# Optimization experiments

Measured on AMD Instinct MI355X. Metric: run time of the kernel, lower is better.

Reference implementation:

```python
import jax, jax.numpy as jnp
import numpy as np

N_NODES = 50000
N_EDGES = 500000
LATENT = 128
MULS = (64, 32, 16)      # multiplicities for l=0,1,2
DIMS = (1, 3, 5)         # 2l+1
FEAT_OFF = (0, 64, 160)  # feature column offset per l
FEAT_DIM = 240
WIG_OFF = (0, 1, 4)      # wigner block offset per l
D_TOT = 9


def _e3nn_linear(x, W0, b0, W1, W2):
    # e3nn Linear: per-l multiplicity mixing, 1/sqrt(mul_in) path norm, bias only on l=0 scalars
    s = x[:, 0:64] @ (W0 / 8.0) + b0                                                   # l=0
    v = jnp.einsum('nmd,mk->nkd', x[:, 64:160].reshape(-1, 32, 3), W1 / jnp.sqrt(32.0)).reshape(-1, 96)
    t = jnp.einsum('nmd,mk->nkd', x[:, 160:240].reshape(-1, 16, 5), W2 / 4.0).reshape(-1, 80)
    return jnp.concatenate([s, v, t], axis=1)


def setup_inputs():
    key = jax.random.key(0)
    ks = iter(jax.random.split(key, 32))
    f32 = jnp.float32
    def lin(i, o):
        return jax.random.normal(next(ks), (i, o), f32) / np.float32(np.sqrt(i))
    inp = {}
    inp['node_features'] = jax.random.normal(next(ks), (N_NODES, FEAT_DIM), f32)
    inp['active_edge_vector'] = jax.random.normal(next(ks), (N_EDGES, 3), f32)
    inp['active_edge_index'] = jax.random.randint(next(ks), (2, N_EDGES), 0, N_NODES)
    inp['wigner_D_all'] = jax.random.normal(next(ks), (N_EDGES, D_TOT, D_TOT), f32)
    # lin_center / lin_neighbor (e3nn Linear per-l weights, scalar bias)
    inp['Wc0'] = lin(64, 64); inp['bc0'] = jnp.zeros((64,), f32)
    inp['Wc1'] = lin(32, 32); inp['Wc2'] = lin(16, 16)
    inp['Wn0'] = lin(64, 64); inp['bn0'] = jnp.zeros((64,), f32)
    inp['Wn1'] = lin(32, 32); inp['Wn2'] = lin(16, 16)
    # sim_linears per l: in_dim = total_mul * (2l+1)
    inp['Ws0'] = lin(64, LATENT);  inp['bs0'] = jnp.zeros((LATENT,), f32)
    inp['Ws1'] = lin(96, LATENT);  inp['bs1'] = jnp.zeros((LATENT,), f32)
    inp['Ws2'] = lin(80, LATENT);  inp['bs2'] = jnp.zeros((LATENT,), f32)
    # final_mlp: Linear(3*LATENT, 2*LATENT) -> SiLU -> Linear(2*LATENT, LATENT)
    inp['Wf1'] = lin(3 * LATENT, 2 * LATENT); inp['bf1'] = jnp.zeros((2 * LATENT,), f32)
    inp['Wf2'] = lin(2 * LATENT, LATENT);     inp['bf2'] = jnp.zeros((LATENT,), f32)
    return inp


def reference(node_features, active_edge_vector, active_edge_index, wigner_D_all,
              Wc0, bc0, Wc1, Wc2, Wn0, bn0, Wn1, Wn2,
              Ws0, bs0, Ws1, bs1, Ws2, bs2, Wf1, bf1, Wf2, bf2):
    # rot_n_feat_ is an exact copy of node_features in the original forward
    center = _e3nn_linear(node_features, Wc0, bc0, Wc1, Wc2)[active_edge_index[0]]    # (E, 240)
    neigh = _e3nn_linear(node_features, Wn0, bn0, Wn1, Wn2)[active_edge_index[1]]     # (E, 240)
    sim_w = ((Ws0, bs0), (Ws1, bs1), (Ws2, bs2))
    latent_list = []
    for l in range(3):
        mul, d, fo = MULS[l], DIMS[l], FEAT_OFF[l]
        cf = center[:, fo:fo + mul * d].reshape(-1, mul, d)   # (E, mul, 2l+1)
        nf = neigh[:, fo:fo + mul * d].reshape(-1, mul, d)
        if l > 0:
            wo = WIG_OFF[l]
            rot = wigner_D_all[:, wo:wo + d, wo:wo + d]       # (E, d, d) per-l wigner block
            cf = jnp.einsum('emd,edq->emq', cf, rot)
            nf = jnp.einsum('emd,edq->emq', nf, rot)
        sim = (cf * nf).reshape(cf.shape[0], -1)              # (E, mul*d)
        W, b = sim_w[l]
        latent_list.append(jax.nn.silu(sim @ W + b))          # (E, LATENT)
    fused = jnp.concatenate(latent_list, axis=1)              # stack(dim=1)+reshape == concat
    h = jax.nn.silu(fused @ Wf1 + bf1)
    return h @ Wf2 + bf2                                      # (E, LATENT)
```

## Files before the change

kernel.cpp:

```cpp
#include <hip/hip_runtime.h>
#include <hip/hip_fp16.h>
#include <math.h>


#define NFEAT 240

typedef _Float16 f16;
typedef _Float16 f16x8 __attribute__((ext_vector_type(8)));
typedef float f32x4 __attribute__((ext_vector_type(4)));

__device__ __forceinline__ float silu_f(float x) {
    return x / (1.0f + __expf(-x));
}

__device__ __forceinline__ int frag_idx(int s, int e, int kk) {
    return ((s * 2 + (e >> 4)) * 64 + (((kk >> 3) << 4) | (e & 15))) * 8 + (kk & 7);
}

template <bool F32>
__global__ void node_kernel(const float* __restrict__ x,
                            const float* __restrict__ Wc0, const float* __restrict__ bc0,
                            const float* __restrict__ Wc1, const float* __restrict__ Wc2,
                            const float* __restrict__ Wn0, const float* __restrict__ bn0,
                            const float* __restrict__ Wn1, const float* __restrict__ Wn2,
                            void* __restrict__ Cp, void* __restrict__ Np,
                            int n_nodes)
{
    int t = blockIdx.x * blockDim.x + threadIdx.x;
    int total = n_nodes * NFEAT;
    if (t >= total) return;
    int n = t / NFEAT;
    int j = t - n * NFEAT;
    const float* xr = x + (size_t)n * NFEAT;
    float ac = 0.f, an = 0.f;
    if (j < 64) {
        #pragma unroll 8
        for (int m = 0; m < 64; ++m) {
            float xv = xr[m];
            ac = fmaf(xv, Wc0[m * 64 + j], ac);
            an = fmaf(xv, Wn0[m * 64 + j], an);
        }
        ac = ac * 0.125f + bc0[j];
        an = an * 0.125f + bn0[j];
    } else if (j < 160) {
        int s = j - 64; int k = s / 3; int d = s - 3 * k;
        #pragma unroll 8
        for (int m = 0; m < 32; ++m) {
            float xv = xr[64 + m * 3 + d];
            ac = fmaf(xv, Wc1[m * 32 + k], ac);
            an = fmaf(xv, Wn1[m * 32 + k], an);
        }
        const float s32 = 0.17677669529663687f;
        ac *= s32; an *= s32;
    } else {
        int s = j - 160; int k = s / 5; int d = s - 5 * k;
        #pragma unroll 8
        for (int m = 0; m < 16; ++m) {
            float xv = xr[160 + m * 5 + d];
            ac = fmaf(xv, Wc2[m * 16 + k], ac);
            an = fmaf(xv, Wn2[m * 16 + k], an);
        }
        ac *= 0.25f; an *= 0.25f;
    }
    if (F32) {
        ((float*)Cp)[t] = ac;
        ((float*)Np)[t] = an;
    } else {
        ((__half*)Cp)[t] = __float2half(ac);
        ((__half*)Np)[t] = __float2half(an);
    }
}

__global__ void pack_kernel(const float* __restrict__ Ws0, const float* __restrict__ Ws1,
                            const float* __restrict__ Ws2, const float* __restrict__ Wf1,
                            const float* __restrict__ Wf2, f16* __restrict__ P)
{
    int idx = blockIdx.x * 256 + threadIdx.x;
    if (idx >= 163840) return;
    int lane = (idx >> 3) & 63;
    int i = idx & 7;
    int kc = ((lane >> 4) << 3) + i;
    int nl = lane & 15;
    float v;
    if (idx < 32768) {
        int fi = idx >> 9; int s = fi >> 3; int nt = fi & 7;
        int l = (s < 2) ? 0 : ((s < 5) ? 1 : 2);
        int s0 = (l == 0) ? 0 : ((l == 1) ? 2 : 5);
        int K = (l == 0) ? 64 : ((l == 1) ? 96 : 80);
        const float* W = (l == 0) ? Ws0 : ((l == 1) ? Ws1 : Ws2);
        int k = (s - s0) * 32 + kc;
        int col = (nt << 4) | nl;
        v = (k < K) ? W[k * 128 + col] : 0.f;
    } else if (idx < 131072) {
        int fi = (idx - 32768) >> 9; int s = fi >> 4; int nt = fi & 15;
        int k = s * 32 + kc;
        int col = (nt << 4) | nl;
        v = Wf1[k * 256 + col];
    } else {
        int fi = (idx - 131072) >> 9; int s = fi >> 3; int nt = fi & 7;
        int k = s * 32 + kc;
        int col = (nt << 4) | nl;
        v = Wf2[k * 128 + col];
    }
    P[idx] = (f16)v;
}

__global__ __launch_bounds__(256, 4) void edge_mfma(
    const f16* __restrict__ C, const f16* __restrict__ Nn,
    const int* __restrict__ eidx, const float* __restrict__ wig,
    const f16* __restrict__ P,
    const float* __restrict__ bs0, const float* __restrict__ bs1,
    const float* __restrict__ bs2, const float* __restrict__ bf1,
    const float* __restrict__ bf2v,
    float* __restrict__ out, int n_edges)
{
    __shared__ __align__(16) f16 latF[24 * 512];
    __shared__ __align__(16) f16 simF[16 * 512];

    const int tid = threadIdx.x;
    const int lane = tid & 63;
    const int w = tid >> 6;
    const long e0 = (long)blockIdx.x * 32;

    {
        int mt = tid >> 7;
        int r = tid & 127;
        int l2 = 32 + (r >> 2);
        int wd = r & 3;
        ((float*)simF)[((14 + mt) * 64 + l2) * 4 + wd] = 0.f;
    }

    #pragma unroll
    for (int it = 0; it < 8; ++it) {
        int t = it * 256 + tid;
        int e = t >> 6, j = t & 63;
        long eg = e0 + e;
        bool a = eg < n_edges;
        int i0 = a ? eidx[eg] : 0;
        int i1 = a ? eidx[(long)n_edges + eg] : 0;
        float c = (float)C[(size_t)i0 * NFEAT + j];
        float n = (float)Nn[(size_t)i1 * NFEAT + j];
        simF[frag_idx(j >> 5, e, j & 31)] = (f16)(c * n);
    }
    #pragma unroll
    for (int it = 0; it < 4; ++it) {
        int t = it * 256 + tid;
        int e = t >> 5, m = t & 31;
        long eg = e0 + e;
        bool a = eg < n_edges;
        int i0 = a ? eidx[eg] : 0;
        int i1 = a ? eidx[(long)n_edges + eg] : 0;
        const float* wg = wig + (a ? eg : 0) * 81;
        int base = 64 + m * 3;
        const f16* cr = C + (size_t)i0 * NFEAT + base;
        const f16* nr = Nn + (size_t)i1 * NFEAT + base;
        float c0 = cr[0], c1 = cr[1], c2 = cr[2];
        float n0 = nr[0], n1 = nr[1], n2 = nr[2];
        #pragma unroll
        for (int q = 0; q < 3; ++q) {
            float r0 = wg[(1 + 0) * 9 + (1 + q)];
            float r1 = wg[(1 + 1) * 9 + (1 + q)];
            float r2 = wg[(1 + 2) * 9 + (1 + q)];
            float cq = c0 * r0 + c1 * r1 + c2 * r2;
            float nq = n0 * r0 + n1 * r1 + n2 * r2;
            int j = base + q;
            simF[frag_idx(j >> 5, e, j & 31)] = (f16)(cq * nq);
        }
    }
    #pragma unroll
    for (int it = 0; it < 2; ++it) {
        int t = it * 256 + tid;
        int e = t >> 4, m = t & 15;
        long eg = e0 + e;
        bool a = eg < n_edges;
        int i0 = a ? eidx[eg] : 0;
        int i1 = a ? eidx[(long)n_edges + eg] : 0;
        const float* wg = wig + (a ? eg : 0) * 81;
        int base = 160 + m * 5;
        const f16* cr = C + (size_t)i0 * NFEAT + base;
        const f16* nr = Nn + (size_t)i1 * NFEAT + base;
        float c[5], n[5];
        #pragma unroll
        for (int d = 0; d < 5; ++d) { c[d] = cr[d]; n[d] = nr[d]; }
        #pragma unroll
        for (int q = 0; q < 5; ++q) {
            float cq = 0.f, nq = 0.f;
            #pragma unroll
            for (int d = 0; d < 5; ++d) {
                float rv = wg[(4 + d) * 9 + (4 + q)];
                cq = fmaf(c[d], rv, cq);
                nq = fmaf(n[d], rv, nq);
            }
            int j = base + q;
            simF[frag_idx(j >> 5, e, j & 31)] = (f16)(cq * nq);
        }
    }
    __syncthreads();

    const f16* WsP  = P;
    const f16* Wf1P = P + 32768;
    const f16* Wf2P = P + 131072;

    {
        const int s0a[3] = {0, 2, 5};
        const int sca[3] = {2, 3, 3};
        const float* bsa[3] = { bs0, bs1, bs2 };
        #pragma unroll
        for (int l = 0; l < 3; ++l) {
            f32x4 a00 = {0.f, 0.f, 0.f, 0.f};
            f32x4 a01 = a00, a10 = a00, a11 = a00;
            #pragma unroll
            for (int s_ = 0; s_ < sca[l]; ++s_) {
                int s = s0a[l] + s_;
                f16x8 A0 = *(const f16x8*)&simF[((s * 2 + 0) * 64 + lane) * 8];
                f16x8 A1 = *(const f16x8*)&simF[((s * 2 + 1) * 64 + lane) * 8];
                f16x8 B0 = *(const f16x8*)&WsP[((s * 8 + 2 * w + 0) * 64 + lane) * 8];
                f16x8 B1 = *(const f16x8*)&WsP[((s * 8 + 2 * w + 1) * 64 + lane) * 8];
                a00 = __builtin_amdgcn_mfma_f32_16x16x32_f16(A0, B0, a00, 0, 0, 0);
                a10 = __builtin_amdgcn_mfma_f32_16x16x32_f16(A1, B0, a10, 0, 0, 0);
                a01 = __builtin_amdgcn_mfma_f32_16x16x32_f16(A0, B1, a01, 0, 0, 0);
                a11 = __builtin_amdgcn_mfma_f32_16x16x32_f16(A1, B1, a11, 0, 0, 0);
            }
            #pragma unroll
            for (int ntl = 0; ntl < 2; ++ntl) {
                int c128 = (2 * w + ntl) * 16 + (lane & 15);
                float bias = bsa[l][c128];
                int n = l * 128 + c128;
                #pragma unroll
                for (int mt = 0; mt < 2; ++mt) {
                    f32x4 av = ntl ? (mt ? a11 : a01) : (mt ? a10 : a00);
                    #pragma unroll
                    for (int r = 0; r < 4; ++r) {
                        int e = mt * 16 + ((lane >> 4) << 2) + r;
                        latF[frag_idx(n >> 5, e, n & 31)] = (f16)silu_f(av[r] + bias);
                    }
                }
            }
        }
    }
    __syncthreads();

    {
        f32x4 acc[2][4];
        #pragma unroll
        for (int mt = 0; mt < 2; ++mt)
            #pragma unroll
            for (int j = 0; j < 4; ++j) {
                f32x4 z = {0.f, 0.f, 0.f, 0.f};
                acc[mt][j] = z;
            }
        for (int s = 0; s < 12; ++s) {
            f16x8 A0 = *(const f16x8*)&latF[((s * 2 + 0) * 64 + lane) * 8];
            f16x8 A1 = *(const f16x8*)&latF[((s * 2 + 1) * 64 + lane) * 8];
            #pragma unroll
            for (int j = 0; j < 4; ++j) {
                f16x8 B = *(const f16x8*)&Wf1P[((s * 16 + 4 * w + j) * 64 + lane) * 8];
                acc[0][j] = __builtin_amdgcn_mfma_f32_16x16x32_f16(A0, B, acc[0][j], 0, 0, 0);
                acc[1][j] = __builtin_amdgcn_mfma_f32_16x16x32_f16(A1, B, acc[1][j], 0, 0, 0);
            }
        }
        #pragma unroll
        for (int j = 0; j < 4; ++j) {
            int col = (4 * w + j) * 16 + (lane & 15);
            float bias = bf1[col];
            #pragma unroll
            for (int mt = 0; mt < 2; ++mt) {
                #pragma unroll
                for (int r = 0; r < 4; ++r) {
                    int e = mt * 16 + ((lane >> 4) << 2) + r;
                    simF[frag_idx(col >> 5, e, col & 31)] = (f16)silu_f(acc[mt][j][r] + bias);
                }
            }
        }
    }
    __syncthreads();

    {
        f32x4 acc[2][2];
        #pragma unroll
        for (int mt = 0; mt < 2; ++mt)
            #pragma unroll
            for (int j = 0; j < 2; ++j) {
                f32x4 z = {0.f, 0.f, 0.f, 0.f};
                acc[mt][j] = z;
            }
        for (int s = 0; s < 8; ++s) {
            f16x8 A0 = *(const f16x8*)&simF[((s * 2 + 0) * 64 + lane) * 8];
            f16x8 A1 = *(const f16x8*)&simF[((s * 2 + 1) * 64 + lane) * 8];
            #pragma unroll
            for (int j = 0; j < 2; ++j) {
                f16x8 B = *(const f16x8*)&Wf2P[((s * 8 + 2 * w + j) * 64 + lane) * 8];
                acc[0][j] = __builtin_amdgcn_mfma_f32_16x16x32_f16(A0, B, acc[0][j], 0, 0, 0);
                acc[1][j] = __builtin_amdgcn_mfma_f32_16x16x32_f16(A1, B, acc[1][j], 0, 0, 0);
            }
        }
        #pragma unroll
        for (int j = 0; j < 2; ++j) {
            int col = (2 * w + j) * 16 + (lane & 15);
            float bias = bf2v[col];
            #pragma unroll
            for (int mt = 0; mt < 2; ++mt) {
                #pragma unroll
                for (int r = 0; r < 4; ++r) {
                    int e = mt * 16 + ((lane >> 4) << 2) + r;
                    long eg = e0 + e;
                    if (eg < n_edges) out[eg * 128 + col] = acc[mt][j][r] + bias;
                }
            }
        }
    }
}

#define EW 6
#define WPB 4
#define EB (EW * WPB)
#define BUFW 260
#define LATW 132

__global__ __launch_bounds__(256, 4) void edge_kernel_f16(
    const void* __restrict__ Cp, const void* __restrict__ Np,
    const int* __restrict__ eidx, const float* __restrict__ wig,
    const float* __restrict__ Ws0, const float* __restrict__ bs0,
    const float* __restrict__ Ws1, const float* __restrict__ bs1,
    const float* __restrict__ Ws2, const float* __restrict__ bs2,
    const float* __restrict__ Wf1, const float* __restrict__ bf1,
    const float* __restrict__ Wf2, const float* __restrict__ bf2v,
    float* __restrict__ out, int n_edges)
{
    __shared__ __align__(16) float bufS[WPB][EW][BUFW];
    __shared__ __align__(16) float latS[WPB][EW][LATW];

    const int w = threadIdx.x >> 6;
    const int lane = threadIdx.x & 63;
    const long e0 = (long)blockIdx.x * EB + (long)w * EW;

    const __half* Chrow[EW];
    const __half* Nhrow[EW];
    bool act[EW];
    #pragma unroll
    for (int e = 0; e < EW; ++e) {
        long eg = e0 + e;
        act[e] = eg < n_edges;
        long i0 = 0, i1 = 0;
        if (act[e]) { i0 = eidx[eg]; i1 = eidx[(long)n_edges + eg]; }
        Chrow[e] = (const __half*)Cp + i0 * NFEAT;
        Nhrow[e] = (const __half*)Np + i1 * NFEAT;
    }
    #define LDC(e, i) (__half2float(Chrow[e][i]))
    #define LDN(e, i) (__half2float(Nhrow[e][i]))

    #pragma unroll
    for (int e = 0; e < EW; ++e) {
        if (act[e]) {
            float c = LDC(e, lane);
            float n = LDN(e, lane);
            bufS[w][e][lane] = c * n;
        }
    }
    #pragma unroll
    for (int it = 0; it < 3; ++it) {
        int t = it * 64 + lane;
        int e = t >> 5;
        int m = t & 31;
        if (act[e]) {
            long eg = e0 + e;
            const float* wg = wig + eg * 81;
            int base = 64 + m * 3;
            float c0 = LDC(e, base + 0), c1 = LDC(e, base + 1), c2 = LDC(e, base + 2);
            float n0 = LDN(e, base + 0), n1 = LDN(e, base + 1), n2 = LDN(e, base + 2);
            #pragma unroll
            for (int q = 0; q < 3; ++q) {
                float r0 = wg[(1 + 0) * 9 + (1 + q)];
                float r1 = wg[(1 + 1) * 9 + (1 + q)];
                float r2 = wg[(1 + 2) * 9 + (1 + q)];
                float cq = c0 * r0 + c1 * r1 + c2 * r2;
                float nq = n0 * r0 + n1 * r1 + n2 * r2;
                bufS[w][e][base + q] = cq * nq;
            }
        }
    }
    #pragma unroll
    for (int it = 0; it < 2; ++it) {
        int t = it * 64 + lane;
        if (t < 96) {
            int e = t >> 4;
            int m = t & 15;
            if (act[e]) {
                long eg = e0 + e;
                const float* wg = wig + eg * 81;
                int base = 160 + m * 5;
                float c[5], n[5];
                #pragma unroll
                for (int d = 0; d < 5; ++d) { c[d] = LDC(e, base + d); n[d] = LDN(e, base + d); }
                #pragma unroll
                for (int q = 0; q < 5; ++q) {
                    float cq = 0.f, nq = 0.f;
                    #pragma unroll
                    for (int d = 0; d < 5; ++d) {
                        float rv = wg[(4 + d) * 9 + (4 + q)];
                        cq = fmaf(c[d], rv, cq);
                        nq = fmaf(n[d], rv, nq);
                    }
                    bufS[w][e][base + q] = cq * nq;
                }
            }
        }
    }
    __builtin_amdgcn_wave_barrier();

    const int k0 = lane * 4;
    float4 hacc[EW];
    {
        float4 hb = *(const float4*)&bf1[k0];
        #pragma unroll
        for (int e = 0; e < EW; ++e) hacc[e] = hb;
    }
    {
        const float* Wsl[3] = { Ws0, Ws1, Ws2 };
        const float* bsl[3] = { bs0, bs1, bs2 };
        const int Kl[3] = { 64, 96, 80 };
        const int offl[3] = { 0, 64, 160 };
        #pragma unroll
        for (int l = 0; l < 3; ++l) {
            const float* W = Wsl[l];
            const int K = Kl[l];
            const int off = offl[l];
            const int c0 = lane * 2;
            float acc0[EW], acc1[EW];
            {
                float b0v = bsl[l][c0];
                float b1v = bsl[l][c0 + 1];
                #pragma unroll
                for (int e = 0; e < EW; ++e) { acc0[e] = b0v; acc1[e] = b1v; }
            }
            for (int i0 = 0; i0 < K; i0 += 4) {
                float2 w0 = *(const float2*)&W[(i0 + 0) * 128 + c0];
                float2 w1 = *(const float2*)&W[(i0 + 1) * 128 + c0];
                float2 w2 = *(const float2*)&W[(i0 + 2) * 128 + c0];
                float2 w3 = *(const float2*)&W[(i0 + 3) * 128 + c0];
                #pragma unroll
                for (int e = 0; e < EW; ++e) {
                    float4 sv = *(const float4*)&bufS[w][e][off + i0];
                    acc0[e] = fmaf(sv.x, w0.x, acc0[e]);
                    acc0[e] = fmaf(sv.y, w1.x, acc0[e]);
                    acc0[e] = fmaf(sv.z, w2.x, acc0[e]);
                    acc0[e] = fmaf(sv.w, w3.x, acc0[e]);
                    acc1[e] = fmaf(sv.x, w0.y, acc1[e]);
                    acc1[e] = fmaf(sv.y, w1.y, acc1[e]);
                    acc1[e] = fmaf(sv.z, w2.y, acc1[e]);
                    acc1[e] = fmaf(sv.w, w3.y, acc1[e]);
                }
            }
            #pragma unroll
            for (int e = 0; e < EW; ++e) {
                float2 lv;
                lv.x = silu_f(acc0[e]);
                lv.y = silu_f(acc1[e]);
                *(float2*)&latS[w][e][c0] = lv;
            }
            __builtin_amdgcn_wave_barrier();

            const float* W1 = Wf1 + (size_t)l * 128 * 256;
            for (int i0 = 0; i0 < 128; i0 += 4) {
                float4 w0 = *(const float4*)&W1[(size_t)(i0 + 0) * 256 + k0];
                float4 w1 = *(const float4*)&W1[(size_t)(i0 + 1) * 256 + k0];
                float4 w2 = *(const float4*)&W1[(size_t)(i0 + 2) * 256 + k0];
                float4 w3 = *(const float4*)&W1[(size_t)(i0 + 3) * 256 + k0];
                #pragma unroll
                for (int e = 0; e < EW; ++e) {
                    float4 lv = *(const float4*)&latS[w][e][i0];
                    hacc[e].x = fmaf(lv.x, w0.x, hacc[e].x); hacc[e].x = fmaf(lv.y, w1.x, hacc[e].x);
                    hacc[e].x = fmaf(lv.z, w2.x, hacc[e].x); hacc[e].x = fmaf(lv.w, w3.x, hacc[e].x);
                    hacc[e].y = fmaf(lv.x, w0.y, hacc[e].y); hacc[e].y = fmaf(lv.y, w1.y, hacc[e].y);
                    hacc[e].y = fmaf(lv.z, w2.y, hacc[e].y); hacc[e].y = fmaf(lv.w, w3.y, hacc[e].y);
                    hacc[e].z = fmaf(lv.x, w0.z, hacc[e].z); hacc[e].z = fmaf(lv.y, w1.z, hacc[e].z);
                    hacc[e].z = fmaf(lv.z, w2.z, hacc[e].z); hacc[e].z = fmaf(lv.w, w3.z, hacc[e].z);
                    hacc[e].w = fmaf(lv.x, w0.w, hacc[e].w); hacc[e].w = fmaf(lv.y, w1.w, hacc[e].w);
                    hacc[e].w = fmaf(lv.z, w2.w, hacc[e].w); hacc[e].w = fmaf(lv.w, w3.w, hacc[e].w);
                }
            }
            __builtin_amdgcn_wave_barrier();
        }
    }
    #pragma unroll
    for (int e = 0; e < EW; ++e) {
        float4 hv;
        hv.x = silu_f(hacc[e].x); hv.y = silu_f(hacc[e].y);
        hv.z = silu_f(hacc[e].z); hv.w = silu_f(hacc[e].w);
        *(float4*)&bufS[w][e][k0] = hv;
    }
    __builtin_amdgcn_wave_barrier();
    {
        int c0 = lane * 2;
        float2 acc[EW];
        float2 bias = *(const float2*)&bf2v[c0];
        #pragma unroll
        for (int e = 0; e < EW; ++e) acc[e] = bias;
        for (int i0 = 0; i0 < 256; i0 += 4) {
            float2 w0 = *(const float2*)&Wf2[(size_t)(i0 + 0) * 128 + c0];
            float2 w1 = *(const float2*)&Wf2[(size_t)(i0 + 1) * 128 + c0];
            float2 w2 = *(const float2*)&Wf2[(size_t)(i0 + 2) * 128 + c0];
            float2 w3 = *(const float2*)&Wf2[(size_t)(i0 + 3) * 128 + c0];
            #pragma unroll
            for (int e = 0; e < EW; ++e) {
                float4 hv = *(const float4*)&bufS[w][e][i0];
                acc[e].x = fmaf(hv.x, w0.x, acc[e].x); acc[e].x = fmaf(hv.y, w1.x, acc[e].x);
                acc[e].x = fmaf(hv.z, w2.x, acc[e].x); acc[e].x = fmaf(hv.w, w3.x, acc[e].x);
                acc[e].y = fmaf(hv.x, w0.y, acc[e].y); acc[e].y = fmaf(hv.y, w1.y, acc[e].y);
                acc[e].y = fmaf(hv.z, w2.y, acc[e].y); acc[e].y = fmaf(hv.w, w3.y, acc[e].y);
            }
        }
        #pragma unroll
        for (int e = 0; e < EW; ++e) {
            long eg = e0 + e;
            if (eg < n_edges) {
                out[eg * 128 + c0 + 0] = acc[e].x;
                out[eg * 128 + c0 + 1] = acc[e].y;
            }
        }
    }
    #undef LDC
    #undef LDN
}

extern "C" void kernel_launch(void* const* d_in, const int* in_sizes, int n_in,
                              void* d_out, int out_size, void* d_ws, size_t ws_size,
                              hipStream_t stream) {
    const float* x    = (const float*)d_in[0];
    const int* eidx   = (const int*)d_in[2];
    const float* wig  = (const float*)d_in[3];
    const float* Wc0  = (const float*)d_in[4];
    const float* bc0  = (const float*)d_in[5];
    const float* Wc1  = (const float*)d_in[6];
    const float* Wc2  = (const float*)d_in[7];
    const float* Wn0  = (const float*)d_in[8];
    const float* bn0  = (const float*)d_in[9];
    const float* Wn1  = (const float*)d_in[10];
    const float* Wn2  = (const float*)d_in[11];
    const float* Ws0  = (const float*)d_in[12];
    const float* bs0  = (const float*)d_in[13];
    const float* Ws1  = (const float*)d_in[14];
    const float* bs1  = (const float*)d_in[15];
    const float* Ws2  = (const float*)d_in[16];
    const float* bs2  = (const float*)d_in[17];
    const float* Wf1  = (const float*)d_in[18];
    const float* bf1  = (const float*)d_in[19];
    const float* Wf2  = (const float*)d_in[20];
    const float* bf2v = (const float*)d_in[21];
    float* out = (float*)d_out;

    const int n_nodes = in_sizes[0] / NFEAT;
    const int n_edges = in_sizes[2] / 2;
    const size_t cn = (size_t)n_nodes * NFEAT;

    const int blkA = 256;
    const int grdA = (int)((cn + blkA - 1) / blkA);

    const size_t needM = cn * 2 * sizeof(__half) + (size_t)163840 * sizeof(f16);

    if (ws_size >= needM) {
        __half* C  = (__half*)d_ws;
        __half* Nh = C + cn;
        f16* P = (f16*)((char*)d_ws + cn * 2 * sizeof(__half));
        node_kernel<false><<<grdA, blkA, 0, stream>>>(x, Wc0, bc0, Wc1, Wc2,
                                                      Wn0, bn0, Wn1, Wn2,
                                                      (void*)C, (void*)Nh, n_nodes);
        pack_kernel<<<640, 256, 0, stream>>>(Ws0, Ws1, Ws2, Wf1, Wf2, P);
        const int grdM = (n_edges + 31) / 32;
        edge_mfma<<<grdM, 256, 0, stream>>>((const f16*)C, (const f16*)Nh,
                                            eidx, wig, P,
                                            bs0, bs1, bs2, bf1, bf2v,
                                            out, n_edges);
    } else {
        __half* C  = (__half*)d_ws;
        __half* Nh = C + cn;
        node_kernel<false><<<grdA, blkA, 0, stream>>>(x, Wc0, bc0, Wc1, Wc2,
                                                      Wn0, bn0, Wn1, Wn2,
                                                      (void*)C, (void*)Nh, n_nodes);
        const int grdB = (n_edges + EB - 1) / EB;
        edge_kernel_f16<<<grdB, 256, 0, stream>>>((const void*)C, (const void*)Nh,
                                                  eidx, wig,
                                                  Ws0, bs0, Ws1, bs1, Ws2, bs2,
                                                  Wf1, bf1, Wf2, bf2v,
                                                  out, n_edges);
    }
}
```

Measured before the change: 1.158 ms.

## Merge node and pack kernels, vectorize l0 gather, swizzle LDS fragments

```diff
diff --git a/kernel.cpp b/kernel.cpp
--- a/kernel.cpp
+++ b/kernel.cpp
@@ -13,22 +13,21 @@
     return x / (1.0f + __expf(-x));
 }
 
-__device__ __forceinline__ int frag_idx(int s, int e, int kk) {
-    return ((s * 2 + (e >> 4)) * 64 + (((kk >> 3) << 4) | (e & 15))) * 8 + (kk & 7);
-}
-
-template <bool F32>
-__global__ void node_kernel(const float* __restrict__ x,
-                            const float* __restrict__ Wc0, const float* __restrict__ bc0,
-                            const float* __restrict__ Wc1, const float* __restrict__ Wc2,
-                            const float* __restrict__ Wn0, const float* __restrict__ bn0,
-                            const float* __restrict__ Wn1, const float* __restrict__ Wn2,
-                            void* __restrict__ Cp, void* __restrict__ Np,
-                            int n_nodes)
+__device__ __forceinline__ int swz_u(int u) { return u ^ ((u >> 3) & 7); }
+
+__device__ __forceinline__ int fidx(int s, int e, int kk) {
+    int u = (s * 2 + (e >> 4)) * 64 + (((kk >> 3) << 4) | (e & 15));
+    return (swz_u(u) << 3) | (kk & 7);
+}
+
+__device__ __forceinline__ void node_compute(
+    const float* __restrict__ x,
+    const float* __restrict__ Wc0, const float* __restrict__ bc0,
+    const float* __restrict__ Wc1, const float* __restrict__ Wc2,
+    const float* __restrict__ Wn0, const float* __restrict__ bn0,
+    const float* __restrict__ Wn1, const float* __restrict__ Wn2,
+    __half* __restrict__ Cp, __half* __restrict__ Np, int t)
 {
-    int t = blockIdx.x * blockDim.x + threadIdx.x;
-    int total = n_nodes * NFEAT;
-    if (t >= total) return;
     int n = t / NFEAT;
     int j = t - n * NFEAT;
     const float* xr = x + (size_t)n * NFEAT;
@@ -62,20 +61,28 @@
         }
         ac *= 0.25f; an *= 0.25f;
     }
-    if (F32) {
-        ((float*)Cp)[t] = ac;
-        ((float*)Np)[t] = an;
-    } else {
-        ((__half*)Cp)[t] = __float2half(ac);
-        ((__half*)Np)[t] = __float2half(an);
-    }
-}
-
-__global__ void pack_kernel(const float* __restrict__ Ws0, const float* __restrict__ Ws1,
+    Cp[t] = __float2half(ac);
+    Np[t] = __float2half(an);
+}
+
+__global__ void prep_kernel(const float* __restrict__ x,
+                            const float* __restrict__ Wc0, const float* __restrict__ bc0,
+                            const float* __restrict__ Wc1, const float* __restrict__ Wc2,
+                            const float* __restrict__ Wn0, const float* __restrict__ bn0,
+                            const float* __restrict__ Wn1, const float* __restrict__ Wn2,
+                            const float* __restrict__ Ws0, const float* __restrict__ Ws1,
                             const float* __restrict__ Ws2, const float* __restrict__ Wf1,
-                            const float* __restrict__ Wf2, f16* __restrict__ P)
+                            const float* __restrict__ Wf2,
+                            __half* __restrict__ Cp, __half* __restrict__ Np,
+                            f16* __restrict__ P, int n_nodes, int grdNode)
 {
-    int idx = blockIdx.x * 256 + threadIdx.x;
+    if (blockIdx.x < (unsigned)grdNode) {
+        int t = blockIdx.x * 256 + threadIdx.x;
+        if (t >= n_nodes * NFEAT) return;
+        node_compute(x, Wc0, bc0, Wc1, Wc2, Wn0, bn0, Wn1, Wn2, Cp, Np, t);
+        return;
+    }
+    int idx = (blockIdx.x - grdNode) * 256 + threadIdx.x;
     if (idx >= 163840) return;
     int lane = (idx >> 3) & 63;
     int i = idx & 7;
@@ -93,14 +100,10 @@
         v = (k < K) ? W[k * 128 + col] : 0.f;
     } else if (idx < 131072) {
         int fi = (idx - 32768) >> 9; int s = fi >> 4; int nt = fi & 15;
-        int k = s * 32 + kc;
-        int col = (nt << 4) | nl;
-        v = Wf1[k * 256 + col];
+        v = Wf1[(s * 32 + kc) * 256 + ((nt << 4) | nl)];
     } else {
         int fi = (idx - 131072) >> 9; int s = fi >> 3; int nt = fi & 7;
-        int k = s * 32 + kc;
-        int col = (nt << 4) | nl;
-        v = Wf2[k * 128 + col];
+        v = Wf2[(s * 32 + kc) * 128 + ((nt << 4) | nl)];
     }
     P[idx] = (f16)v;
 }
@@ -116,31 +119,35 @@
 {
     __shared__ __align__(16) f16 latF[24 * 512];
     __shared__ __align__(16) f16 simF[16 * 512];
+    __shared__ int i0s[32], i1s[32];
 
     const int tid = threadIdx.x;
     const int lane = tid & 63;
+    const int laneS = lane ^ ((lane >> 3) & 7);
     const int w = tid >> 6;
     const long e0 = (long)blockIdx.x * 32;
 
-    {
-        int mt = tid >> 7;
-        int r = tid & 127;
-        int l2 = 32 + (r >> 2);
-        int wd = r & 3;
-        ((float*)simF)[((14 + mt) * 64 + l2) * 4 + wd] = 0.f;
-    }
-
-    #pragma unroll
-    for (int it = 0; it < 8; ++it) {
-        int t = it * 256 + tid;
-        int e = t >> 6, j = t & 63;
-        long eg = e0 + e;
+    if (tid < 32) {
+        long eg = e0 + tid;
         bool a = eg < n_edges;
-        int i0 = a ? eidx[eg] : 0;
-        int i1 = a ? eidx[(long)n_edges + eg] : 0;
-        float c = (float)C[(size_t)i0 * NFEAT + j];
-        float n = (float)Nn[(size_t)i1 * NFEAT + j];
-        simF[frag_idx(j >> 5, e, j & 31)] = (f16)(c * n);
+        i0s[tid] = a ? eidx[eg] : 0;
+        i1s[tid] = a ? eidx[(long)n_edges + eg] : 0;
+    }
+    {
+        int ul = tid >> 2;
+        int u = (14 + (ul >> 5)) * 64 + 32 + (ul & 31);
+        ((float*)simF)[(swz_u(u) << 2) + (tid & 3)] = 0.f;
+    }
+    __syncthreads();
+
+    {
+        int e = tid >> 3, kg = tid & 7;
+        int i0 = i0s[e], i1 = i1s[e];
+        f16x8 cv = *(const f16x8*)&C[(size_t)i0 * NFEAT + kg * 8];
+        f16x8 nv = *(const f16x8*)&Nn[(size_t)i1 * NFEAT + kg * 8];
+        f16x8 p = cv * nv;
+        int u = ((kg >> 2) * 2 + (e >> 4)) * 64 + ((kg & 3) << 4) + (e & 15);
+        *(f16x8*)&simF[swz_u(u) << 3] = p;
     }
     #pragma unroll
     for (int it = 0; it < 4; ++it) {
@@ -148,12 +155,10 @@
         int e = t >> 5, m = t & 31;
         long eg = e0 + e;
         bool a = eg < n_edges;
-        int i0 = a ? eidx[eg] : 0;
-        int i1 = a ? eidx[(long)n_edges + eg] : 0;
         const float* wg = wig + (a ? eg : 0) * 81;
         int base = 64 + m * 3;
-        const f16* cr = C + (size_t)i0 * NFEAT + base;
-        const f16* nr = Nn + (size_t)i1 * NFEAT + base;
+        const f16* cr = C + (size_t)i0s[e] * NFEAT + base;
+        const f16* nr = Nn + (size_t)i1s[e] * NFEAT + base;
         float c0 = cr[0], c1 = cr[1], c2 = cr[2];
         float n0 = nr[0], n1 = nr[1], n2 = nr[2];
         #pragma unroll
@@ -164,7 +169,7 @@
             float cq = c0 * r0 + c1 * r1 + c2 * r2;
             float nq = n0 * r0 + n1 * r1 + n2 * r2;
             int j = base + q;
-            simF[frag_idx(j >> 5, e, j & 31)] = (f16)(cq * nq);
+            simF[fidx(j >> 5, e, j & 31)] = (f16)(cq * nq);
         }
     }
     #pragma unroll
@@ -173,12 +178,10 @@
         int e = t >> 4, m = t & 15;
         long eg = e0 + e;
         bool a = eg < n_edges;
-        int i0 = a ? eidx[eg] : 0;
-        int i1 = a ? eidx[(long)n_edges + eg] : 0;
         const float* wg = wig + (a ? eg : 0) * 81;
         int base = 160 + m * 5;
-        const f16* cr = C + (size_t)i0 * NFEAT + base;
-        const f16* nr = Nn + (size_t)i1 * NFEAT + base;
+        const f16* cr = C + (size_t)i0s[e] * NFEAT + base;
+        const f16* nr = Nn + (size_t)i1s[e] * NFEAT + base;
         float c[5], n[5];
         #pragma unroll
         for (int d = 0; d < 5; ++d) { c[d] = cr[d]; n[d] = nr[d]; }
@@ -192,7 +195,7 @@
                 nq = fmaf(n[d], rv, nq);
             }
             int j = base + q;
-            simF[frag_idx(j >> 5, e, j & 31)] = (f16)(cq * nq);
+            simF[fidx(j >> 5, e, j & 31)] = (f16)(cq * nq);
         }
     }
     __syncthreads();
@@ -212,8 +215,8 @@
             #pragma unroll
             for (int s_ = 0; s_ < sca[l]; ++s_) {
                 int s = s0a[l] + s_;
-                f16x8 A0 = *(const f16x8*)&simF[((s * 2 + 0) * 64 + lane) * 8];
-                f16x8 A1 = *(const f16x8*)&simF[((s * 2 + 1) * 64 + lane) * 8];
+                f16x8 A0 = *(const f16x8*)&simF[(((s * 2 + 0) * 64 + laneS)) * 8];
+                f16x8 A1 = *(const f16x8*)&simF[(((s * 2 + 1) * 64 + laneS)) * 8];
                 f16x8 B0 = *(const f16x8*)&WsP[((s * 8 + 2 * w + 0) * 64 + lane) * 8];
                 f16x8 B1 = *(const f16x8*)&WsP[((s * 8 + 2 * w + 1) * 64 + lane) * 8];
                 a00 = __builtin_amdgcn_mfma_f32_16x16x32_f16(A0, B0, a00, 0, 0, 0);
@@ -232,7 +235,7 @@
                     #pragma unroll
                     for (int r = 0; r < 4; ++r) {
                         int e = mt * 16 + ((lane >> 4) << 2) + r;
-                        latF[frag_idx(n >> 5, e, n & 31)] = (f16)silu_f(av[r] + bias);
+                        latF[fidx(n >> 5, e, n & 31)] = (f16)silu_f(av[r] + bias);
                     }
                 }
             }
@@ -250,8 +253,8 @@
                 acc[mt][j] = z;
             }
         for (int s = 0; s < 12; ++s) {
-            f16x8 A0 = *(const f16x8*)&latF[((s * 2 + 0) * 64 + lane) * 8];
-            f16x8 A1 = *(const f16x8*)&latF[((s * 2 + 1) * 64 + lane) * 8];
+            f16x8 A0 = *(const f16x8*)&latF[(((s * 2 + 0) * 64 + laneS)) * 8];
+            f16x8 A1 = *(const f16x8*)&latF[(((s * 2 + 1) * 64 + laneS)) * 8];
             #pragma unroll
             for (int j = 0; j < 4; ++j) {
                 f16x8 B = *(const f16x8*)&Wf1P[((s * 16 + 4 * w + j) * 64 + lane) * 8];
@@ -268,7 +271,7 @@
                 #pragma unroll
                 for (int r = 0; r < 4; ++r) {
                     int e = mt * 16 + ((lane >> 4) << 2) + r;
-                    simF[frag_idx(col >> 5, e, col & 31)] = (f16)silu_f(acc[mt][j][r] + bias);
+                    simF[fidx(col >> 5, e, col & 31)] = (f16)silu_f(acc[mt][j][r] + bias);
                 }
             }
         }
@@ -285,8 +288,8 @@
                 acc[mt][j] = z;
             }
         for (int s = 0; s < 8; ++s) {
-            f16x8 A0 = *(const f16x8*)&simF[((s * 2 + 0) * 64 + lane) * 8];
-            f16x8 A1 = *(const f16x8*)&simF[((s * 2 + 1) * 64 + lane) * 8];
+            f16x8 A0 = *(const f16x8*)&simF[(((s * 2 + 0) * 64 + laneS)) * 8];
+            f16x8 A1 = *(const f16x8*)&simF[(((s * 2 + 1) * 64 + laneS)) * 8];
             #pragma unroll
             for (int j = 0; j < 2; ++j) {
                 f16x8 B = *(const f16x8*)&Wf2P[((s * 8 + 2 * w + j) * 64 + lane) * 8];
@@ -309,6 +312,19 @@
             }
         }
     }
+}
+
+__global__ void node_kernel_fb(const float* __restrict__ x,
+                               const float* __restrict__ Wc0, const float* __restrict__ bc0,
+                               const float* __restrict__ Wc1, const float* __restrict__ Wc2,
+                               const float* __restrict__ Wn0, const float* __restrict__ bn0,
+                               const float* __restrict__ Wn1, const float* __restrict__ Wn2,
+                               __half* __restrict__ Cp, __half* __restrict__ Np,
+                               int n_nodes)
+{
+    int t = blockIdx.x * blockDim.x + threadIdx.x;
+    if (t >= n_nodes * NFEAT) return;
+    node_compute(x, Wc0, bc0, Wc1, Wc2, Wn0, bn0, Wn1, Wn2, Cp, Np, t);
 }
 
 #define EW 6
@@ -553,19 +569,17 @@
     const int n_edges = in_sizes[2] / 2;
     const size_t cn = (size_t)n_nodes * NFEAT;
 
-    const int blkA = 256;
-    const int grdA = (int)((cn + blkA - 1) / blkA);
-
+    const int grdA = (int)((cn + 255) / 256);
     const size_t needM = cn * 2 * sizeof(__half) + (size_t)163840 * sizeof(f16);
 
     if (ws_size >= needM) {
         __half* C  = (__half*)d_ws;
         __half* Nh = C + cn;
         f16* P = (f16*)((char*)d_ws + cn * 2 * sizeof(__half));
-        node_kernel<false><<<grdA, blkA, 0, stream>>>(x, Wc0, bc0, Wc1, Wc2,
-                                                      Wn0, bn0, Wn1, Wn2,
-                                                      (void*)C, (void*)Nh, n_nodes);
-        pack_kernel<<<640, 256, 0, stream>>>(Ws0, Ws1, Ws2, Wf1, Wf2, P);
+        prep_kernel<<<grdA + 640, 256, 0, stream>>>(x, Wc0, bc0, Wc1, Wc2,
+                                                    Wn0, bn0, Wn1, Wn2,
+                                                    Ws0, Ws1, Ws2, Wf1, Wf2,
+                                                    C, Nh, P, n_nodes, grdA);
         const int grdM = (n_edges + 31) / 32;
         edge_mfma<<<grdM, 256, 0, stream>>>((const f16*)C, (const f16*)Nh,
                                             eidx, wig, P,
@@ -574,9 +588,9 @@
     } else {
         __half* C  = (__half*)d_ws;
         __half* Nh = C + cn;
-        node_kernel<false><<<grdA, blkA, 0, stream>>>(x, Wc0, bc0, Wc1, Wc2,
-                                                      Wn0, bn0, Wn1, Wn2,
-                                                      (void*)C, (void*)Nh, n_nodes);
+        node_kernel_fb<<<grdA, 256, 0, stream>>>(x, Wc0, bc0, Wc1, Wc2,
+                                                 Wn0, bn0, Wn1, Wn2,
+                                                 C, Nh, n_nodes);
         const int grdB = (n_edges + EB - 1) / EB;
         edge_kernel_f16<<<grdB, 256, 0, stream>>>((const void*)C, (const void*)Nh,
                                                   eidx, wig,
```

New measurement: 1.038 ms. 10.4% less time.
